# Optimization experiments

Measured on AMD Instinct MI355X. Metric: run time of the kernel, lower is better.

Reference implementation:

```python
import jax, jax.numpy as jnp
import numpy as np

B, N, M, D_MODEL, D_K, D_V = 8, 2048, 2048, 1024, 1024, 1024
NEG = -1000000000.0


def setup_inputs() -> dict:
    key = jax.random.key(0)
    ks = jax.random.split(key, 10)
    s = 1.0 / np.sqrt(D_MODEL)
    return {
        "querys": jax.random.normal(ks[0], (B, N, D_MODEL), jnp.float32),
        "keys": jax.random.normal(ks[1], (B, M, D_MODEL), jnp.float32),
        "values": jax.random.normal(ks[2], (B, M, D_MODEL), jnp.float32),
        "mask": jax.random.randint(ks[3], (N, M), 0, 2, jnp.int32),
        "Wq": jax.random.normal(ks[4], (D_K, D_MODEL), jnp.float32) * s,
        "bq": jnp.zeros((D_K,), jnp.float32),
        "Wk": jax.random.normal(ks[5], (D_K, D_MODEL), jnp.float32) * s,
        "bk": jnp.zeros((D_K,), jnp.float32),
        "Wv": jax.random.normal(ks[6], (D_V, D_MODEL), jnp.float32) * s,
        "bv": jnp.zeros((D_V,), jnp.float32),
    }


def reference(querys, keys, values, mask, Wq, bq, Wk, bk, Wv, bv):
    # Linear projections (torch Linear: x @ W.T + b)
    q = querys @ Wq.T + bq          # [B, N, Dk]
    k = keys @ Wk.T + bk            # [B, M, Dk]
    v = values @ Wv.T + bv          # [B, M, Dv]
    # Original computes QK^T via broadcast mul+sum; GEMM form is identical math.
    # NOTE: no 1/sqrt(d) scaling, matching the source.
    scores = jnp.einsum('bnd,bmd->bnm', q, k)  # [B, N, M]
    scores = jnp.where(mask[None, :, :] == 0, NEG, scores)
    weights = jax.nn.softmax(scores, axis=2)
    out = jnp.einsum('bnm,bmd->bnd', weights, v)  # [B, N, Dv]
    return out
```

## Files before the change

### kernel.cpp

```cpp
#include <hip/hip_runtime.h>
#include <cstdint>

typedef __bf16 bf16_t;
typedef __bf16 bf16x8 __attribute__((ext_vector_type(8)));
typedef float f32x4 __attribute__((ext_vector_type(4)));

#define AS1 __attribute__((address_space(1)))
#define AS3 __attribute__((address_space(3)))

__device__ __forceinline__ void gload_lds16(const bf16_t* g, bf16_t* l) {
    __builtin_amdgcn_global_load_lds((const AS1 void*)g, (AS3 void*)l, 16, 0, 0);
}
__device__ __forceinline__ f32x4 mfma_bf16(bf16x8 a, bf16x8 b, f32x4 c) {
    return __builtin_amdgcn_mfma_f32_16x16x32_bf16(a, b, c, 0, 0, 0);
}

template <bool SPLIT, int BIAS, int OUTMODE>
__global__ __launch_bounds__(512, 2) void gemm256(
    const bf16_t* __restrict__ Ah, const bf16_t* __restrict__ Al, long long strideA, int lda,
    const bf16_t* __restrict__ Bh, const bf16_t* __restrict__ Bl, long long strideB, int ldb,
    void* __restrict__ C0, void* __restrict__ C1, long long strideC, int ldc,
    const float* __restrict__ bias, int K, int zrows)
{
    __shared__ bf16_t lds[4 * 16384];

    int bx = blockIdx.x, by = blockIdx.y, bz = blockIdx.z;
    {
        const int gx = gridDim.x, gy = gridDim.y, gz = gridDim.z;
        const int n = gx * gy * gz;
        if ((n & 7) == 0) {
            int lin = bx + gx * (by + gy * bz);
            lin = (lin & 7) * (n >> 3) + (lin >> 3);
            bx = lin % gx; lin /= gx;
            by = lin % gy; bz = lin / gy;
        }
    }

    const int rowBase = by * 256;
    const int colBase = bx * 256;
    const bf16_t* AhB = Ah + (long long)bz * strideA;
    const bf16_t* BhB = Bh + (long long)bz * strideB;
    const bf16_t* AlB = SPLIT ? Al + (long long)bz * strideA : nullptr;
    const bf16_t* BlB = SPLIT ? Bl + (long long)bz * strideB : nullptr;

    const int t = threadIdx.x;
    const int lane = t & 63;
    const int w = t >> 6;
    const int wm = w >> 2;
    const int wn = w & 3;

    const int r0 = t >> 2;
    const int sl8 = ((t & 3) ^ ((r0 >> 1) & 3)) * 8;
    const long long aoff0 = (long long)(rowBase + r0) * lda + sl8;
    const long long aoff1 = (long long)(rowBase + r0 + 128) * lda + sl8;
    const long long boff0 = (long long)(colBase + r0) * ldb + sl8;
    const long long boff1 = (long long)(colBase + r0 + 128) * ldb + sl8;

    const int NT = SPLIT ? (K >> 5) * 3 : (K >> 5);

    auto tsrc = [&](int jt, const bf16_t*& sA, const bf16_t*& sB, long long& k0) {
        if (SPLIT) {
            const int chunk = jt / 3;
            const int term = jt - chunk * 3;
            k0 = (long long)chunk * 32;
            sA = (term == 2) ? AlB : AhB;
            sB = (term == 1) ? BlB : BhB;
        } else {
            k0 = (long long)jt * 32;
            sA = AhB; sB = BhB;
        }
    };

    auto stage = [&](int jt) {
        const bf16_t *sA, *sB; long long k0;
        tsrc(jt, sA, sB, k0);
        bf16_t* db = lds + (jt & 3) * 16384;
        gload_lds16(sA + aoff0 + k0, db + t * 8);
        gload_lds16(sA + aoff1 + k0, db + 4096 + t * 8);
        gload_lds16(sB + boff0 + k0, db + 8192 + t * 8);
        gload_lds16(sB + boff1 + k0, db + 12288 + t * 8);
    };

    f32x4 acc[8][4] = {};

    stage(0); stage(1); stage(2);
    asm volatile("s_waitcnt vmcnt(8)" ::: "memory");
    __builtin_amdgcn_s_barrier();

    const int fr = lane & 15;
    const int kqs = ((lane >> 4) ^ ((lane >> 1) & 3)) * 8;

    for (int j = 0; j < NT; ++j) {
        const bf16_t* bufA = lds + (j & 3) * 16384;
        const bf16_t* bufB = bufA + 8192;

        if (j + 3 < NT) stage(j + 3);

        bf16x8 a[8], b[4];
#pragma unroll
        for (int mi = 0; mi < 8; mi++)
            a[mi] = *(const bf16x8*)&bufA[(wm * 128 + mi * 16 + fr) * 32 + kqs];
#pragma unroll
        for (int ni = 0; ni < 4; ni++)
            b[ni] = *(const bf16x8*)&bufB[(wn * 64 + ni * 16 + fr) * 32 + kqs];

#pragma unroll
        for (int mi = 0; mi < 8; mi++)
#pragma unroll
            for (int ni = 0; ni < 4; ni++)
                acc[mi][ni] = mfma_bf16(a[mi], b[ni], acc[mi][ni]);

        if (j + 1 < NT) {
            if (j < NT - 3)       asm volatile("s_waitcnt vmcnt(8)" ::: "memory");
            else if (j == NT - 3) asm volatile("s_waitcnt vmcnt(4)" ::: "memory");
            else                  asm volatile("s_waitcnt vmcnt(0)" ::: "memory");
            __builtin_amdgcn_s_barrier();
        }
    }

    const int fc = lane & 15;
    const int fr4 = (lane >> 4) * 4;

    if (OUTMODE == 3) {
        const int zb = rowBase / zrows;
        const int mBase = rowBase - zb * zrows;
#pragma unroll
        for (int mi = 0; mi < 8; mi++)
#pragma unroll
            for (int ni = 0; ni < 4; ni++) {
                const int m0 = mBase + wm * 128 + mi * 16 + fr4;
                const int col = colBase + wn * 64 + ni * 16 + fc;
                bf16_t q[4];
#pragma unroll
                for (int rg = 0; rg < 4; rg++) {
                    float v = acc[mi][ni][rg];
                    if (BIAS == 1) v += bias[col];
                    q[rg] = (bf16_t)v;
                }
                const long long off = (long long)zb * strideC + (long long)col * ldc + m0;
                *(ushort4*)&((bf16_t*)C0)[off] = *(const ushort4*)q;
            }
        return;
    }

#pragma unroll
    for (int mi = 0; mi < 8; mi++)
#pragma unroll
        for (int ni = 0; ni < 4; ni++)
#pragma unroll
            for (int rg = 0; rg < 4; rg++) {
                const int row = rowBase + wm * 128 + mi * 16 + fr4 + rg;
                const int col = colBase + wn * 64 + ni * 16 + fc;
                float v = acc[mi][ni][rg];
                if (BIAS == 1) v += bias[col];
                else if (BIAS == 2) v += bias[row];
                const long long off = (long long)bz * strideC + (long long)row * ldc + col;
                if (OUTMODE == 0) {
                    ((float*)C0)[off] = v;
                } else if (OUTMODE == 1) {
                    ((bf16_t*)C0)[off] = (bf16_t)v;
                } else {
                    const bf16_t h = (bf16_t)v;
                    ((bf16_t*)C0)[off] = h;
                    ((bf16_t*)C1)[off] = (bf16_t)(v - (float)h);
                }
            }
}

__global__ __launch_bounds__(256) void split_f32(const float* __restrict__ x,
                                                 bf16_t* __restrict__ h,
                                                 bf16_t* __restrict__ l)
{
    const long long i = ((long long)blockIdx.x * 256 + threadIdx.x) * 4;
    const float4 v = *(const float4*)&x[i];
    bf16_t hh[4], ll[4];
    const float vv[4] = {v.x, v.y, v.z, v.w};
#pragma unroll
    for (int j = 0; j < 4; j++) {
        hh[j] = (bf16_t)vv[j];
        ll[j] = (bf16_t)(vv[j] - (float)hh[j]);
    }
    *(short4*)&h[i] = *(short4*)hh;
    *(short4*)&l[i] = *(short4*)ll;
}

__global__ __launch_bounds__(256) void cast_f32(const float* __restrict__ x,
                                                bf16_t* __restrict__ y)
{
    const long long i = ((long long)blockIdx.x * 256 + threadIdx.x) * 4;
    const float4 v = *(const float4*)&x[i];
    bf16_t hh[4] = {(bf16_t)v.x, (bf16_t)v.y, (bf16_t)v.z, (bf16_t)v.w};
    *(short4*)&y[i] = *(short4*)hh;
}

__global__ __launch_bounds__(256) void prep_weights(
    const float* __restrict__ Wq, const float* __restrict__ Wk, const float* __restrict__ Wv,
    bf16_t* __restrict__ WqH, bf16_t* __restrict__ WqL,
    bf16_t* __restrict__ WkH, bf16_t* __restrict__ WkL, bf16_t* __restrict__ WvB)
{
    const long long i = ((long long)blockIdx.x * 256 + threadIdx.x) * 4;
    const int sel = blockIdx.y;
    const float* x = (sel == 0) ? Wq : (sel == 1) ? Wk : Wv;
    const float4 v = *(const float4*)&x[i];
    const float vv[4] = {v.x, v.y, v.z, v.w};
    bf16_t hh[4], ll[4];
#pragma unroll
    for (int j = 0; j < 4; j++) {
        hh[j] = (bf16_t)vv[j];
        ll[j] = (bf16_t)(vv[j] - (float)hh[j]);
    }
    if (sel == 0) { *(short4*)&WqH[i] = *(short4*)hh; *(short4*)&WqL[i] = *(short4*)ll; }
    else if (sel == 1) { *(short4*)&WkH[i] = *(short4*)hh; *(short4*)&WkL[i] = *(short4*)ll; }
    else { *(short4*)&WvB[i] = *(short4*)hh; }
}

__global__ __launch_bounds__(256) void pack_mask(const int* __restrict__ mask,
                                                 unsigned char* __restrict__ mp)
{
    const long long i = (long long)blockIdx.x * 256 + threadIdx.x;
    const int4 a = *(const int4*)&mask[i * 8];
    const int4 b = *(const int4*)&mask[i * 8 + 4];
    unsigned int v = 0;
    v |= (a.x != 0) ? 1u : 0u;  v |= (a.y != 0) ? 2u : 0u;
    v |= (a.z != 0) ? 4u : 0u;  v |= (a.w != 0) ? 8u : 0u;
    v |= (b.x != 0) ? 16u : 0u; v |= (b.y != 0) ? 32u : 0u;
    v |= (b.z != 0) ? 64u : 0u; v |= (b.w != 0) ? 128u : 0u;
    mp[i] = (unsigned char)v;
}

__global__ __launch_bounds__(256) void softmax_rows(const float* __restrict__ S,
                                                    bf16_t* __restrict__ P,
                                                    const unsigned char* __restrict__ mp,
                                                    int n0)
{
    __shared__ float red[4];
    const long long r = blockIdx.x;
    const float* row = S + r * 2048;
    const int t = threadIdx.x;

    const float4 s0 = *(const float4*)&row[t * 8];
    const float4 s1 = *(const float4*)&row[t * 8 + 4];
    const unsigned int mb = mp[(long long)(n0 + (int)(r & 2047)) * 256 + t];

    float v[8] = {s0.x, s0.y, s0.z, s0.w, s1.x, s1.y, s1.z, s1.w};
#pragma unroll
    for (int i = 0; i < 8; i++) v[i] = ((mb >> i) & 1u) ? v[i] : -1000000000.0f;

    float m = v[0];
#pragma unroll
    for (int i = 1; i < 8; i++) m = fmaxf(m, v[i]);
#pragma unroll
    for (int off = 32; off; off >>= 1) m = fmaxf(m, __shfl_xor(m, off));
    if ((t & 63) == 0) red[t >> 6] = m;
    __syncthreads();
    const float rowmax = fmaxf(fmaxf(red[0], red[1]), fmaxf(red[2], red[3]));
    __syncthreads();

    float sum = 0.0f;
    float e[8];
#pragma unroll
    for (int i = 0; i < 8; i++) { e[i] = __expf(v[i] - rowmax); sum += e[i]; }
#pragma unroll
    for (int off = 32; off; off >>= 1) sum += __shfl_xor(sum, off);
    if ((t & 63) == 0) red[t >> 6] = sum;
    __syncthreads();
    const float inv = 1.0f / (red[0] + red[1] + red[2] + red[3]);

    bf16_t e8[8];
#pragma unroll
    for (int i = 0; i < 8; i++) e8[i] = (bf16_t)(e[i] * inv);
    *(bf16x8*)&P[r * 2048 + t * 8] = *(const bf16x8*)e8;
}

extern "C" void kernel_launch(void* const* d_in, const int* in_sizes, int n_in,
                              void* d_out, int out_size, void* d_ws, size_t ws_size,
                              hipStream_t stream) {
    constexpr int Bb = 8, N = 2048, M = 2048, D = 1024;
    constexpr long long MB = 1LL << 20;

    const float* querys = (const float*)d_in[0];
    const float* keys   = (const float*)d_in[1];
    const float* values = (const float*)d_in[2];
    const int*   mask   = (const int*)d_in[3];
    const float* Wq = (const float*)d_in[4];
    const float* bq = (const float*)d_in[5];
    const float* Wk = (const float*)d_in[6];
    const float* bk = (const float*)d_in[7];
    const float* Wv = (const float*)d_in[8];
    const float* bv = (const float*)d_in[9];
    float* out = (float*)d_out;

    const long long w = (long long)ws_size;
    auto needB = [&](long long cb) { return 11 * MB + cb * 52 * MB; };
    int CB = 0;
    if      (w >= needB(8)) CB = 8;
    else if (w >= needB(4)) CB = 4;
    else if (w >= needB(2)) CB = 2;
    else if (w >= needB(1)) CB = 1;
    const bool batched = (CB != 0);
    int NCH = N;
    if (!batched) {
        CB = 1;
        NCH = (w >= 39 * MB + 512 * 2048 * 6) ? 512 : 256;
    }

    char* ws = (char*)d_ws;
    long long o = 0;
    auto carve = [&](long long bytes) { char* p = ws + o; o += bytes; return p; };
    bf16_t* WqH = (bf16_t*)carve(2 * MB);
    bf16_t* WqL = (bf16_t*)carve(2 * MB);
    bf16_t* WkH = (bf16_t*)carve(2 * MB);
    bf16_t* WkL = (bf16_t*)carve(2 * MB);
    bf16_t* WvB = (bf16_t*)carve(2 * MB);
    unsigned char* MP = (unsigned char*)carve(((long long)N * M / 8 + 4095) & ~4095LL);
    bf16_t* XH  = (bf16_t*)carve((long long)CB * 4 * MB);
    bf16_t* XL  = (bf16_t*)carve((long long)CB * 4 * MB);
    bf16_t* QH  = (bf16_t*)carve((long long)CB * 4 * MB);
    bf16_t* QL  = (bf16_t*)carve((long long)CB * 4 * MB);
    bf16_t* KH  = (bf16_t*)carve((long long)CB * 4 * MB);
    bf16_t* KL  = (bf16_t*)carve((long long)CB * 4 * MB);
    bf16_t* VT  = (bf16_t*)carve((long long)CB * 4 * MB);
    float*  S   = (float*)carve(batched ? (long long)CB * N * M * 4 : (long long)NCH * 2048 * 4);
    bf16_t* P   = (bf16_t*)carve(batched ? (long long)CB * N * M * 2 : (long long)NCH * 2048 * 2);

    dim3 blk(256), blkG(512);
    const long long grpElems = (long long)CB * N * D;

    prep_weights<<<dim3((D * D) / 1024, 3), blk, 0, stream>>>(
        Wq, Wk, Wv, WqH, WqL, WkH, WkL, WvB);
    pack_mask<<<dim3((N * (long long)M / 8) / 256), blk, 0, stream>>>(mask, MP);

    for (int b0 = 0; b0 < Bb; b0 += CB) {
        const long long xoff = (long long)b0 * N * D;
        split_f32<<<dim3(grpElems / 1024), blk, 0, stream>>>(querys + xoff, XH, XL);
        gemm256<true, 1, 2><<<dim3(D / 256, CB * N / 256, 1), blkG, 0, stream>>>(
            XH, XL, 0, D, WqH, WqL, 0, D, QH, QL, 0, D, bq, D, 1);
        split_f32<<<dim3(grpElems / 1024), blk, 0, stream>>>(keys + xoff, XH, XL);
        gemm256<true, 1, 2><<<dim3(D / 256, CB * M / 256, 1), blkG, 0, stream>>>(
            XH, XL, 0, D, WkH, WkL, 0, D, KH, KL, 0, D, bk, D, 1);
        cast_f32<<<dim3(grpElems / 1024), blk, 0, stream>>>(values + xoff, XH);
        gemm256<false, 1, 3><<<dim3(D / 256, CB * M / 256, 1), blkG, 0, stream>>>(
            XH, nullptr, 0, D, WvB, nullptr, 0, D,
            VT, nullptr, (long long)D * M, M, bv, D, M);

        if (batched) {
            gemm256<true, 0, 0><<<dim3(M / 256, N / 256, CB), blkG, 0, stream>>>(
                QH, QL, (long long)N * D, D,
                KH, KL, (long long)M * D, D,
                S, nullptr, (long long)N * M, M, nullptr, D, 1);
            softmax_rows<<<dim3(CB * N), blk, 0, stream>>>(S, P, MP, 0);
            gemm256<false, 0, 0><<<dim3(D / 256, N / 256, CB), blkG, 0, stream>>>(
                P, nullptr, (long long)N * M, M,
                VT, nullptr, (long long)D * M, M,
                out + xoff, nullptr, (long long)N * D, D, nullptr, M, 1);
        } else {
            for (int z = 0; z < CB; z++) {
                for (int n0 = 0; n0 < N; n0 += NCH) {
                    gemm256<true, 0, 0><<<dim3(M / 256, NCH / 256, 1), blkG, 0, stream>>>(
                        QH + ((long long)z * N + n0) * D, QL + ((long long)z * N + n0) * D, 0, D,
                        KH + (long long)z * M * D, KL + (long long)z * M * D, 0, D,
                        S, nullptr, 0, M, nullptr, D, 1);
                    softmax_rows<<<dim3(NCH), blk, 0, stream>>>(S, P, MP, n0);
                    gemm256<false, 0, 0><<<dim3(D / 256, NCH / 256, 1), blkG, 0, stream>>>(
                        P, nullptr, 0, M, VT + (long long)z * D * M, nullptr, 0, M,
                        out + ((long long)(b0 + z) * N + n0) * D, nullptr, 0, D, nullptr, M, 1);
                }
            }
        }
    }
    (void)in_sizes; (void)n_in; (void)out_size;
}
```

Before: 1.007 ms.

## Add dedicated 128x128 split-bf16 GEMM that loads hi/lo tiles together per K-chunk

Adds a separate kernel for the three-term split-bf16 GEMMs (Q/K projections and QK^T). It uses 128x128 tiles with 256 threads and stages the A-hi, A-lo, B-hi and B-lo tiles together for each 32-wide K chunk. Within a chunk it reuses the a0/b0 register fragments across the three product terms, instead of streaming each term as a separate K-step that reloads the hi tiles. The old 256x256 kernel is kept, specialised to the single-term bf16 GEMMs. In exchange, the new kernel has smaller tiles with lower arithmetic intensity, only double buffering, and a full vmcnt(0) wait plus barrier every iteration, which may hide memory latency less well.

```diff
diff --git a/kernel.cpp b/kernel.cpp
--- a/kernel.cpp
+++ b/kernel.cpp
@@ -15,14 +15,14 @@
     return __builtin_amdgcn_mfma_f32_16x16x32_bf16(a, b, c, 0, 0, 0);
 }
 
-template <bool SPLIT, int BIAS, int OUTMODE>
-__global__ __launch_bounds__(512, 2) void gemm256(
+template <int BIAS, int OUTMODE>
+__global__ __launch_bounds__(256) void gemm_sp(
     const bf16_t* __restrict__ Ah, const bf16_t* __restrict__ Al, long long strideA, int lda,
     const bf16_t* __restrict__ Bh, const bf16_t* __restrict__ Bl, long long strideB, int ldb,
     void* __restrict__ C0, void* __restrict__ C1, long long strideC, int ldc,
-    const float* __restrict__ bias, int K, int zrows)
-{
-    __shared__ bf16_t lds[4 * 16384];
+    const float* __restrict__ bias, int K)
+{
+    __shared__ bf16_t lds[2 * 16384];
 
     int bx = blockIdx.x, by = blockIdx.y, bz = blockIdx.z;
     {
@@ -36,12 +36,138 @@
         }
     }
 
+    const int rowBase = by * 128;
+    const int colBase = bx * 128;
+    const bf16_t* AhB = Ah + (long long)bz * strideA;
+    const bf16_t* BhB = Bh + (long long)bz * strideB;
+    const bf16_t* AlB = Al + (long long)bz * strideA;
+    const bf16_t* BlB = Bl + (long long)bz * strideB;
+
+    const int t = threadIdx.x;
+    const int lane = t & 63;
+    const int w = t >> 6;
+    const int wr = (w >> 1) * 64;
+    const int wc = (w & 1) * 64;
+
+    const int r0 = t >> 2;
+    const int sl8 = ((t & 3) ^ ((r0 >> 1) & 3)) * 8;
+    const long long aoff0 = (long long)(rowBase + r0) * lda + sl8;
+    const long long aoff1 = (long long)(rowBase + r0 + 64) * lda + sl8;
+    const long long boff0 = (long long)(colBase + r0) * ldb + sl8;
+    const long long boff1 = (long long)(colBase + r0 + 64) * ldb + sl8;
+
+    const int NC = K >> 5;
+
+    auto stage = [&](int c) {
+        bf16_t* db = lds + (c & 1) * 16384;
+        const long long k0 = (long long)c * 32;
+        gload_lds16(AhB + aoff0 + k0, db + t * 8);
+        gload_lds16(AhB + aoff1 + k0, db + 2048 + t * 8);
+        gload_lds16(AlB + aoff0 + k0, db + 4096 + t * 8);
+        gload_lds16(AlB + aoff1 + k0, db + 6144 + t * 8);
+        gload_lds16(BhB + boff0 + k0, db + 8192 + t * 8);
+        gload_lds16(BhB + boff1 + k0, db + 10240 + t * 8);
+        gload_lds16(BlB + boff0 + k0, db + 12288 + t * 8);
+        gload_lds16(BlB + boff1 + k0, db + 14336 + t * 8);
+    };
+
+    f32x4 acc[4][4] = {};
+
+    stage(0);
+    asm volatile("s_waitcnt vmcnt(0)" ::: "memory");
+    __builtin_amdgcn_s_barrier();
+
+    const int fr = lane & 15;
+    const int kqs = ((lane >> 4) ^ ((lane >> 1) & 3)) * 8;
+
+    for (int c = 0; c < NC; ++c) {
+        const bf16_t* base = lds + (c & 1) * 16384;
+
+        if (c + 1 < NC) stage(c + 1);
+
+        bf16x8 a0[4], a1[4], b0[4], b1[4];
+#pragma unroll
+        for (int mi = 0; mi < 4; mi++)
+            a0[mi] = *(const bf16x8*)&base[(wr + mi * 16 + fr) * 32 + kqs];
+#pragma unroll
+        for (int ni = 0; ni < 4; ni++)
+            b0[ni] = *(const bf16x8*)&base[8192 + (wc + ni * 16 + fr) * 32 + kqs];
+#pragma unroll
+        for (int mi = 0; mi < 4; mi++)
+#pragma unroll
+            for (int ni = 0; ni < 4; ni++)
+                acc[mi][ni] = mfma_bf16(a0[mi], b0[ni], acc[mi][ni]);
+#pragma unroll
+        for (int ni = 0; ni < 4; ni++)
+            b1[ni] = *(const bf16x8*)&base[12288 + (wc + ni * 16 + fr) * 32 + kqs];
+#pragma unroll
+        for (int mi = 0; mi < 4; mi++)
+#pragma unroll
+            for (int ni = 0; ni < 4; ni++)
+                acc[mi][ni] = mfma_bf16(a0[mi], b1[ni], acc[mi][ni]);
+#pragma unroll
+        for (int mi = 0; mi < 4; mi++)
+            a1[mi] = *(const bf16x8*)&base[4096 + (wr + mi * 16 + fr) * 32 + kqs];
+#pragma unroll
+        for (int mi = 0; mi < 4; mi++)
+#pragma unroll
+            for (int ni = 0; ni < 4; ni++)
+                acc[mi][ni] = mfma_bf16(a1[mi], b0[ni], acc[mi][ni]);
+
+        if (c + 1 < NC) {
+            asm volatile("s_waitcnt vmcnt(0)" ::: "memory");
+            __builtin_amdgcn_s_barrier();
+        }
+    }
+
+    const int fc = lane & 15;
+    const int fr4 = (lane >> 4) * 4;
+#pragma unroll
+    for (int mi = 0; mi < 4; mi++)
+#pragma unroll
+        for (int ni = 0; ni < 4; ni++)
+#pragma unroll
+            for (int rg = 0; rg < 4; rg++) {
+                const int row = rowBase + wr + mi * 16 + fr4 + rg;
+                const int col = colBase + wc + ni * 16 + fc;
+                float v = acc[mi][ni][rg];
+                if (BIAS == 1) v += bias[col];
+                const long long off = (long long)bz * strideC + (long long)row * ldc + col;
+                if (OUTMODE == 0) {
+                    ((float*)C0)[off] = v;
+                } else {
+                    const bf16_t h = (bf16_t)v;
+                    ((bf16_t*)C0)[off] = h;
+                    ((bf16_t*)C1)[off] = (bf16_t)(v - (float)h);
+                }
+            }
+}
+
+template <int BIAS, int OUTMODE>
+__global__ __launch_bounds__(512, 2) void gemm256(
+    const bf16_t* __restrict__ A, long long strideA, int lda,
+    const bf16_t* __restrict__ B, long long strideB, int ldb,
+    void* __restrict__ C0, long long strideC, int ldc,
+    const float* __restrict__ bias, int K, int zrows)
+{
+    __shared__ bf16_t lds[4 * 16384];
+
+    int bx = blockIdx.x, by = blockIdx.y, bz = blockIdx.z;
+    {
+        const int gx = gridDim.x, gy = gridDim.y, gz = gridDim.z;
+        const int n = gx * gy * gz;
+        if ((n & 7) == 0) {
+            int lin = bx + gx * (by + gy * bz);
+            lin = (lin & 7) * (n >> 3) + (lin >> 3);
+            bx = lin % gx; lin /= gx;
+            by = lin % gy; bz = lin / gy;
+        }
+    }
+
     const int rowBase = by * 256;
     const int colBase = bx * 256;
-    const bf16_t* AhB = Ah + (long long)bz * strideA;
-    const bf16_t* BhB = Bh + (long long)bz * strideB;
-    const bf16_t* AlB = SPLIT ? Al + (long long)bz * strideA : nullptr;
-    const bf16_t* BlB = SPLIT ? Bl + (long long)bz * strideB : nullptr;
+    const bf16_t* AB = A + (long long)bz * strideA;
+    const bf16_t* BB = B + (long long)bz * strideB;
 
     const int t = threadIdx.x;
     const int lane = t & 63;
@@ -56,29 +182,15 @@
     const long long boff0 = (long long)(colBase + r0) * ldb + sl8;
     const long long boff1 = (long long)(colBase + r0 + 128) * ldb + sl8;
 
-    const int NT = SPLIT ? (K >> 5) * 3 : (K >> 5);
-
-    auto tsrc = [&](int jt, const bf16_t*& sA, const bf16_t*& sB, long long& k0) {
-        if (SPLIT) {
-            const int chunk = jt / 3;
-            const int term = jt - chunk * 3;
-            k0 = (long long)chunk * 32;
-            sA = (term == 2) ? AlB : AhB;
-            sB = (term == 1) ? BlB : BhB;
-        } else {
-            k0 = (long long)jt * 32;
-            sA = AhB; sB = BhB;
-        }
-    };
+    const int NT = K >> 5;
 
     auto stage = [&](int jt) {
-        const bf16_t *sA, *sB; long long k0;
-        tsrc(jt, sA, sB, k0);
+        const long long k0 = (long long)jt * 32;
         bf16_t* db = lds + (jt & 3) * 16384;
-        gload_lds16(sA + aoff0 + k0, db + t * 8);
-        gload_lds16(sA + aoff1 + k0, db + 4096 + t * 8);
-        gload_lds16(sB + boff0 + k0, db + 8192 + t * 8);
-        gload_lds16(sB + boff1 + k0, db + 12288 + t * 8);
+        gload_lds16(AB + aoff0 + k0, db + t * 8);
+        gload_lds16(AB + aoff1 + k0, db + 4096 + t * 8);
+        gload_lds16(BB + boff0 + k0, db + 8192 + t * 8);
+        gload_lds16(BB + boff1 + k0, db + 12288 + t * 8);
     };
 
     f32x4 acc[8][4] = {};
@@ -153,17 +265,8 @@
                 const int col = colBase + wn * 64 + ni * 16 + fc;
                 float v = acc[mi][ni][rg];
                 if (BIAS == 1) v += bias[col];
-                else if (BIAS == 2) v += bias[row];
                 const long long off = (long long)bz * strideC + (long long)row * ldc + col;
-                if (OUTMODE == 0) {
-                    ((float*)C0)[off] = v;
-                } else if (OUTMODE == 1) {
-                    ((bf16_t*)C0)[off] = (bf16_t)v;
-                } else {
-                    const bf16_t h = (bf16_t)v;
-                    ((bf16_t*)C0)[off] = h;
-                    ((bf16_t*)C1)[off] = (bf16_t)(v - (float)h);
-                }
+                ((float*)C0)[off] = v;
             }
 }
 
@@ -333,37 +436,37 @@
     for (int b0 = 0; b0 < Bb; b0 += CB) {
         const long long xoff = (long long)b0 * N * D;
         split_f32<<<dim3(grpElems / 1024), blk, 0, stream>>>(querys + xoff, XH, XL);
-        gemm256<true, 1, 2><<<dim3(D / 256, CB * N / 256, 1), blkG, 0, stream>>>(
-            XH, XL, 0, D, WqH, WqL, 0, D, QH, QL, 0, D, bq, D, 1);
+        gemm_sp<1, 2><<<dim3(D / 128, CB * N / 128, 1), blk, 0, stream>>>(
+            XH, XL, 0, D, WqH, WqL, 0, D, QH, QL, 0, D, bq, D);
         split_f32<<<dim3(grpElems / 1024), blk, 0, stream>>>(keys + xoff, XH, XL);
-        gemm256<true, 1, 2><<<dim3(D / 256, CB * M / 256, 1), blkG, 0, stream>>>(
-            XH, XL, 0, D, WkH, WkL, 0, D, KH, KL, 0, D, bk, D, 1);
+        gemm_sp<1, 2><<<dim3(D / 128, CB * M / 128, 1), blk, 0, stream>>>(
+            XH, XL, 0, D, WkH, WkL, 0, D, KH, KL, 0, D, bk, D);
         cast_f32<<<dim3(grpElems / 1024), blk, 0, stream>>>(values + xoff, XH);
-        gemm256<false, 1, 3><<<dim3(D / 256, CB * M / 256, 1), blkG, 0, stream>>>(
-            XH, nullptr, 0, D, WvB, nullptr, 0, D,
-            VT, nullptr, (long long)D * M, M, bv, D, M);
+        gemm256<1, 3><<<dim3(D / 256, CB * M / 256, 1), blkG, 0, stream>>>(
+            XH, 0, D, WvB, 0, D,
+            VT, (long long)D * M, M, bv, D, M);
 
         if (batched) {
-            gemm256<true, 0, 0><<<dim3(M / 256, N / 256, CB), blkG, 0, stream>>>(
+            gemm_sp<0, 0><<<dim3(M / 128, N / 128, CB), blk, 0, stream>>>(
                 QH, QL, (long long)N * D, D,
                 KH, KL, (long long)M * D, D,
-                S, nullptr, (long long)N * M, M, nullptr, D, 1);
+                S, nullptr, (long long)N * M, M, nullptr, D);
             softmax_rows<<<dim3(CB * N), blk, 0, stream>>>(S, P, MP, 0);
-            gemm256<false, 0, 0><<<dim3(D / 256, N / 256, CB), blkG, 0, stream>>>(
-                P, nullptr, (long long)N * M, M,
-                VT, nullptr, (long long)D * M, M,
-                out + xoff, nullptr, (long long)N * D, D, nullptr, M, 1);
+            gemm256<0, 0><<<dim3(D / 256, N / 256, CB), blkG, 0, stream>>>(
+                P, (long long)N * M, M,
+                VT, (long long)D * M, M,
+                out + xoff, (long long)N * D, D, nullptr, M, 1);
         } else {
             for (int z = 0; z < CB; z++) {
                 for (int n0 = 0; n0 < N; n0 += NCH) {
-                    gemm256<true, 0, 0><<<dim3(M / 256, NCH / 256, 1), blkG, 0, stream>>>(
+                    gemm_sp<0, 0><<<dim3(M / 128, NCH / 128, 1), blk, 0, stream>>>(
                         QH + ((long long)z * N + n0) * D, QL + ((long long)z * N + n0) * D, 0, D,
                         KH + (long long)z * M * D, KL + (long long)z * M * D, 0, D,
-                        S, nullptr, 0, M, nullptr, D, 1);
+                        S, nullptr, 0, M, nullptr, D);
                     softmax_rows<<<dim3(NCH), blk, 0, stream>>>(S, P, MP, n0);
-                    gemm256<false, 0, 0><<<dim3(D / 256, NCH / 256, 1), blkG, 0, stream>>>(
-                        P, nullptr, 0, M, VT + (long long)z * D * M, nullptr, 0, M,
-                        out + ((long long)(b0 + z) * N + n0) * D, nullptr, 0, D, nullptr, M, 1);
+                    gemm256<0, 0><<<dim3(D / 256, NCH / 256, 1), blkG, 0, stream>>>(
+                        P, 0, M, VT + (long long)z * D * M, 0, M,
+                        out + ((long long)(b0 + z) * N + n0) * D, 0, D, nullptr, M, 1);
                 }
             }
         }
```

Measured after the change: 858.7 us. 1.17x faster.
